# Optimization experiments

Hardware: AMD Instinct MI355X
Metric: run time of the kernel (lower is better)

Reference implementation:

```python
import jax, jax.numpy as jnp
import numpy as np
import math

B, H, T, DH, D = 1, 8, 2048, 64, 64
NEG_INF = -1e30
EPS = 1e-9

def setup_inputs() -> dict:
    key = jax.random.key(0)
    ks = jax.random.split(key, 6)
    q = jax.random.normal(ks[0], (B, H, T, DH), dtype=jnp.float32)
    k = jax.random.normal(ks[1], (B, H, T, DH), dtype=jnp.float32)
    v = jax.random.normal(ks[2], (B, H, T, DH), dtype=jnp.float32)
    edge_type_bias = 0.1 * jax.random.normal(ks[3], (4,), dtype=jnp.float32)
    neigh_idx = jax.random.randint(ks[4], (H, T, D), 0, T).astype(jnp.int32)
    edge_type = jax.random.randint(ks[5], (H, T, D), 0, 5).astype(jnp.int32)
    return {"q": q, "k": k, "v": v, "edge_type_bias": edge_type_bias,
            "neigh_idx": neigh_idx, "edge_type": edge_type}

def _masked_softmax(scores, mask):
    # scores: [B,H,T,D] fp32, mask: [1,H,T,D] bool; zeros on all-masked rows
    masked = jnp.where(mask, scores, NEG_INF)
    m = jnp.max(masked, axis=-1, keepdims=True)
    e = jnp.where(mask, jnp.exp(masked - m), 0.0)
    denom = jnp.maximum(jnp.sum(e, axis=-1, keepdims=True), EPS)
    return e / denom

def reference(q, k, v, edge_type_bias, neigh_idx, edge_type):
    Bq, Hq, Tq, dh = q.shape
    # safe_neighbor_idx: clamp to valid range
    s_idx = jnp.clip(neigh_idx, 0, Tq - 1)                       # [H,T,D]
    # causal_neighbor_mask: valid (>=0) and neighbor <= query position
    pos = jnp.arange(Tq, dtype=neigh_idx.dtype)[None, :, None]    # [1,T,1]
    mask = (neigh_idx >= 0) & (neigh_idx <= pos)                  # [H,T,D]
    # edge-type bias: type 0 -> no bias, types 1..4 -> learnable bias
    full_bias = jnp.concatenate([jnp.zeros((1,), jnp.float32),
                                 edge_type_bias.astype(jnp.float32)])
    bias_htd = full_bias[edge_type]                               # [H,T,D]
    # gather neighbor K/V: k_g[b,h,t,n,:] = k[b,h,s_idx[h,t,n],:]
    h_ix = jnp.arange(Hq)[:, None, None]                          # [H,1,1]
    k_g = k[:, h_ix, s_idx]                                       # [B,H,T,D,dh]
    v_g = v[:, h_ix, s_idx]                                       # [B,H,T,D,dh]
    scores = jnp.einsum('bhtc,bhtnc->bhtn',
                        q.astype(jnp.float32),
                        k_g.astype(jnp.float32)) / math.sqrt(dh)
    scores = scores + bias_htd[None]                              # [B,H,T,D]
    w = _masked_softmax(scores, mask[None])                       # [B,H,T,D]
    y = jnp.einsum('bhtn,bhtnc->bhtc', w, v_g.astype(jnp.float32))
    return y.astype(v.dtype)
```

## Files before the change

### kernel.cpp

```cpp
#include <hip/hip_runtime.h>
#include <hip/hip_fp16.h>

constexpr int H  = 8;
constexpr int T  = 2048;
constexpr int DH = 64;
constexpr int D  = 64;
constexpr int NKV = H * T * DH;

typedef _Float16 half2v __attribute__((ext_vector_type(2)));

#if defined(__has_builtin)
#if __has_builtin(__builtin_amdgcn_fdot2)
#define HAVE_FDOT2 1
#endif
#if __has_builtin(__builtin_amdgcn_permlane32_swap)
#define HAVE_PL32 1
#endif
#if __has_builtin(__builtin_amdgcn_permlane16_swap)
#define HAVE_PL16 1
#endif
#endif

__device__ __forceinline__ float dot2acc(half2v a, half2v b, float c) {
#ifdef HAVE_FDOT2
    return __builtin_amdgcn_fdot2(a, b, c, false);
#else
    return c + (float)a.x * (float)b.x + (float)a.y * (float)b.y;
#endif
}

__device__ __forceinline__ half2v h2bits(int b) { return __builtin_bit_cast(half2v, b); }

__device__ __forceinline__ half2v f2h2(float x, float y) {
    __half2 h = __float22half2_rn(make_float2(x, y));
    return __builtin_bit_cast(half2v, h);
}

template<int CTRL>
__device__ __forceinline__ float dpp_mov_f(float x) {
    int yi = __builtin_amdgcn_update_dpp(0, __builtin_bit_cast(int, x),
                                         CTRL, 0xF, 0xF, true);
    return __builtin_bit_cast(float, yi);
}
template<int CTRL>
__device__ __forceinline__ float dpp_add_f(float x) { return x + dpp_mov_f<CTRL>(x); }
template<int CTRL>
__device__ __forceinline__ float dpp_max_f(float x) { return fmaxf(x, dpp_mov_f<CTRL>(x)); }

__device__ __forceinline__ float xor32add_f(float x) {
#ifdef HAVE_PL32
    unsigned u = __builtin_bit_cast(unsigned, x);
    auto r = __builtin_amdgcn_permlane32_swap(u, u, false, false);
    return __builtin_bit_cast(float, (unsigned)r[0]) + __builtin_bit_cast(float, (unsigned)r[1]);
#else
    return x + __shfl_xor(x, 32);
#endif
}
__device__ __forceinline__ float xor32max_f(float x) {
#ifdef HAVE_PL32
    unsigned u = __builtin_bit_cast(unsigned, x);
    auto r = __builtin_amdgcn_permlane32_swap(u, u, false, false);
    return fmaxf(__builtin_bit_cast(float, (unsigned)r[0]), __builtin_bit_cast(float, (unsigned)r[1]));
#else
    return fmaxf(x, __shfl_xor(x, 32));
#endif
}
__device__ __forceinline__ float xor16add_f(float x) {
#ifdef HAVE_PL16
    unsigned u = __builtin_bit_cast(unsigned, x);
    auto r = __builtin_amdgcn_permlane16_swap(u, u, false, false);
    return __builtin_bit_cast(float, (unsigned)r[0]) + __builtin_bit_cast(float, (unsigned)r[1]);
#else
    return x + __shfl_xor(x, 16);
#endif
}
__device__ __forceinline__ float xor16max_f(float x) {
#ifdef HAVE_PL16
    unsigned u = __builtin_bit_cast(unsigned, x);
    auto r = __builtin_amdgcn_permlane16_swap(u, u, false, false);
    return fmaxf(__builtin_bit_cast(float, (unsigned)r[0]), __builtin_bit_cast(float, (unsigned)r[1]));
#else
    return fmaxf(x, __shfl_xor(x, 16));
#endif
}
__device__ __forceinline__ half2v xor32add_h2(half2v x) {
#ifdef HAVE_PL32
    unsigned u = __builtin_bit_cast(unsigned, x);
    auto r = __builtin_amdgcn_permlane32_swap(u, u, false, false);
    return h2bits((int)r[0]) + h2bits((int)r[1]);
#else
    return x + h2bits(__shfl_xor(__builtin_bit_cast(int, x), 32));
#endif
}
__device__ __forceinline__ half2v xor16add_h2(half2v x) {
#ifdef HAVE_PL16
    unsigned u = __builtin_bit_cast(unsigned, x);
    auto r = __builtin_amdgcn_permlane16_swap(u, u, false, false);
    return h2bits((int)r[0]) + h2bits((int)r[1]);
#else
    return x + h2bits(__shfl_xor(__builtin_bit_cast(int, x), 16));
#endif
}
__device__ __forceinline__ half2v xor8add_h2(half2v x) {
    return x + h2bits(__shfl_xor(__builtin_bit_cast(int, x), 8));
}

__global__ __launch_bounds__(256) void cvt_f32_f16(
    const float* __restrict__ k, const float* __restrict__ v,
    __half* __restrict__ kh, __half* __restrict__ vh)
{
    const int i = (blockIdx.x * 256 + threadIdx.x) * 8;
    const float* src = (blockIdx.y == 0) ? k : v;
    __half*      dst = (blockIdx.y == 0) ? kh : vh;
    const float4 a = *reinterpret_cast<const float4*>(src + i);
    const float4 b = *reinterpret_cast<const float4*>(src + i + 4);
    __half2 hh[4];
    hh[0] = __float22half2_rn(make_float2(a.x, a.y));
    hh[1] = __float22half2_rn(make_float2(a.z, a.w));
    hh[2] = __float22half2_rn(make_float2(b.x, b.y));
    hh[3] = __float22half2_rn(make_float2(b.z, b.w));
    *reinterpret_cast<float4*>(dst + i) = *reinterpret_cast<const float4*>(hh);
}

__global__ __launch_bounds__(256) void wayfinder_attn_f16(
    const float* __restrict__ q,
    const __half* __restrict__ kh,
    const __half* __restrict__ vh,
    const float* __restrict__ eb,
    const int*   __restrict__ nidx,
    const int*   __restrict__ etyp,
    float* __restrict__ out)
{
    const int wave = threadIdx.x >> 6;
    const int lane = threadIdx.x & 63;
    const int bid  = blockIdx.x;
    const int work = ((bid & 7) << 9) | (bid >> 3);
    const int flat = (work << 2) + wave;
    const int h    = flat >> 11;
    const int t    = flat & (T - 1);
    const int grp  = lane >> 3;
    const int sub  = lane & 7;

    const long long rowoff = (long long)flat * DH;
    const int*      nrow   = nidx + (long long)flat * D;
    const int*      erow   = etyp + (long long)flat * D;

    const int4 i0 = *reinterpret_cast<const int4*>(nrow + grp * 8);
    const int4 i1 = *reinterpret_cast<const int4*>(nrow + grp * 8 + 4);
    const int4 e0 = *reinterpret_cast<const int4*>(erow + grp * 8);
    const int4 e1 = *reinterpret_cast<const int4*>(erow + grp * 8 + 4);

    const float4 qa = *reinterpret_cast<const float4*>(q + rowoff + sub * 8);
    const float4 qb = *reinterpret_cast<const float4*>(q + rowoff + sub * 8 + 4);

    const int idx_i[8] = {i0.x, i0.y, i0.z, i0.w, i1.x, i1.y, i1.z, i1.w};
    const int et_i [8] = {e0.x, e0.y, e0.z, e0.w, e1.x, e1.y, e1.z, e1.w};

    const __half* khead = kh + (long long)h * T * DH;
    const __half* vhead = vh + (long long)h * T * DH;

    int s_i[8];
    int mskbits = 0;
    #pragma unroll
    for (int i = 0; i < 8; ++i) {
        const bool mk = (unsigned)idx_i[i] <= (unsigned)t;
        s_i[i] = mk ? idx_i[i] : 0;
        mskbits |= mk ? (1 << i) : 0;
    }

    float4 kf[8], vf[8];
    #pragma unroll
    for (int i = 0; i < 8; ++i) {
        const long long ro = (long long)s_i[i] * DH + sub * 8;
        kf[i] = *reinterpret_cast<const float4*>(khead + ro);
        vf[i] = *reinterpret_cast<const float4*>(vhead + ro);
    }

    const float4 ebv = *reinterpret_cast<const float4*>(eb);
    float bias_i[8];
    #pragma unroll
    for (int i = 0; i < 8; ++i) {
        const int et = et_i[i];
        bias_i[i] = (et == 1) ? ebv.x : (et == 2) ? ebv.y :
                    (et == 3) ? ebv.z : (et == 4) ? ebv.w : 0.0f;
    }

    half2v qp[4];
    qp[0] = f2h2(qa.x, qa.y);
    qp[1] = f2h2(qa.z, qa.w);
    qp[2] = f2h2(qb.x, qb.y);
    qp[3] = f2h2(qb.z, qb.w);

    float sc[8];
    #pragma unroll
    for (int i = 0; i < 8; ++i) {
        const half2v* kp = reinterpret_cast<const half2v*>(&kf[i]);
        float p = dot2acc(qp[0], kp[0],
                  dot2acc(qp[1], kp[1],
                  dot2acc(qp[2], kp[2],
                  dot2acc(qp[3], kp[3], 0.0f))));
        p = dpp_add_f<0xB1>(p);
        p = dpp_add_f<0x4E>(p);
        p = dpp_add_f<0x141>(p);
        sc[i] = p;
    }

    float masked[8];
    float mx = -1e30f;
    #pragma unroll
    for (int i = 0; i < 8; ++i) {
        const bool mk = (mskbits >> i) & 1;
        masked[i] = mk ? fmaf(sc[i], 0.125f, bias_i[i]) : -1e30f;
        mx = fmaxf(mx, masked[i]);
    }
    mx = dpp_max_f<0x140>(mx);
    mx = xor16max_f(mx);
    mx = xor32max_f(mx);

    float e[8];
    float sum = 0.0f;
    #pragma unroll
    for (int i = 0; i < 8; ++i) {
        const bool mk = (mskbits >> i) & 1;
        e[i] = mk ? __expf(masked[i] - mx) : 0.0f;
        sum += e[i];
    }
    sum = dpp_add_f<0x140>(sum);
    sum = xor16add_f(sum);
    sum = xor32add_f(sum);
    const float rden = 1.0f / fmaxf(sum, 1e-9f);

    float acc[8] = {0.f, 0.f, 0.f, 0.f, 0.f, 0.f, 0.f, 0.f};
    #pragma unroll
    for (int i = 0; i < 8; ++i) {
        const float w = e[i] * rden;
        const half2v* vp = reinterpret_cast<const half2v*>(&vf[i]);
        acc[0] += w * (float)vp[0].x;  acc[1] += w * (float)vp[0].y;
        acc[2] += w * (float)vp[1].x;  acc[3] += w * (float)vp[1].y;
        acc[4] += w * (float)vp[2].x;  acc[5] += w * (float)vp[2].y;
        acc[6] += w * (float)vp[3].x;  acc[7] += w * (float)vp[3].y;
    }

    half2v h0 = f2h2(acc[0], acc[1]);
    half2v h1 = f2h2(acc[2], acc[3]);
    half2v h2 = f2h2(acc[4], acc[5]);
    half2v h3 = f2h2(acc[6], acc[7]);
    h0 = xor8add_h2(h0);  h1 = xor8add_h2(h1);
    h2 = xor8add_h2(h2);  h3 = xor8add_h2(h3);
    h0 = xor16add_h2(h0); h1 = xor16add_h2(h1);
    h2 = xor16add_h2(h2); h3 = xor16add_h2(h3);
    h0 = xor32add_h2(h0); h1 = xor32add_h2(h1);
    h2 = xor32add_h2(h2); h3 = xor32add_h2(h3);

    if (lane < 16) {
        const int s8   = (lane & 7) * 8;
        const int half = lane >> 3;
        const float4 o = half
            ? make_float4((float)h2.x, (float)h2.y, (float)h3.x, (float)h3.y)
            : make_float4((float)h0.x, (float)h0.y, (float)h1.x, (float)h1.y);
        *reinterpret_cast<float4*>(out + rowoff + s8 + half * 4) = o;
    }
}

__global__ __launch_bounds__(256) void wayfinder_attn_f32(
    const float* __restrict__ q, const float* __restrict__ k,
    const float* __restrict__ v, const float* __restrict__ eb,
    const int* __restrict__ nidx, const int* __restrict__ etyp,
    float* __restrict__ out)
{
    const int wave = threadIdx.x >> 6;
    const int lane = threadIdx.x & 63;
    const int flat = (blockIdx.x << 2) + wave;
    const int h    = flat >> 11;
    const int t    = flat & (T - 1);
    const int grp  = lane >> 4;
    const int sub  = lane & 15;

    __shared__ int    sidx[4][64];
    __shared__ float  ssc [4][64];
    __shared__ float2 swv [4][64];

    const long long rowoff = (long long)flat * DH;
    const long long noff = (long long)flat * D + lane;
    const int  idx = nidx[noff];
    const int  et  = etyp[noff];
    const int  s   = min(max(idx, 0), T - 1);
    const bool msk = (idx >= 0) && (idx <= t);
    const float4 ebv  = *reinterpret_cast<const float4*>(eb);
    const float  bias = (et == 1) ? ebv.x : (et == 2) ? ebv.y :
                        (et == 3) ? ebv.z : (et == 4) ? ebv.w : 0.0f;
    sidx[wave][lane] = s;
    const float4 qf = *reinterpret_cast<const float4*>(q + rowoff + sub * 4);
    __syncthreads();

    const float* khead = k + (long long)h * T * DH;
    #pragma unroll
    for (int i = 0; i < 16; ++i) {
        const int n  = i * 4 + grp;
        const int sn = sidx[wave][n];
        const float4 kf = *reinterpret_cast<const float4*>(khead + sn * DH + sub * 4);
        float p = qf.x * kf.x + qf.y * kf.y + qf.z * kf.z + qf.w * kf.w;
        p += __shfl_xor(p, 1);
        p += __shfl_xor(p, 2);
        p += __shfl_xor(p, 4);
        p += __shfl_xor(p, 8);
        if (sub == 0) ssc[wave][n] = p;
    }
    __syncthreads();

    const float sc     = ssc[wave][lane];
    const float masked = msk ? (sc * 0.125f + bias) : -1e30f;
    float mx = masked;
    #pragma unroll
    for (int off = 32; off > 0; off >>= 1) mx = fmaxf(mx, __shfl_xor(mx, off));
    const float e = msk ? __expf(masked - mx) : 0.0f;
    float sum = e;
    #pragma unroll
    for (int off = 32; off > 0; off >>= 1) sum += __shfl_xor(sum, off);
    const float w = e / fmaxf(sum, 1e-9f);
    swv[wave][lane] = make_float2(w, __int_as_float(s));
    __syncthreads();

    const float* vhead = v + (long long)h * T * DH;
    float4 acc = make_float4(0.f, 0.f, 0.f, 0.f);
    #pragma unroll
    for (int i = 0; i < 16; ++i) {
        const int    n  = i * 4 + grp;
        const float2 ws = swv[wave][n];
        const int    sn = __float_as_int(ws.y);
        const float4 vf = *reinterpret_cast<const float4*>(vhead + sn * DH + sub * 4);
        acc.x += ws.x * vf.x; acc.y += ws.x * vf.y;
        acc.z += ws.x * vf.z; acc.w += ws.x * vf.w;
    }
    #pragma unroll
    for (int off = 16; off <= 32; off <<= 1) {
        acc.x += __shfl_xor(acc.x, off); acc.y += __shfl_xor(acc.y, off);
        acc.z += __shfl_xor(acc.z, off); acc.w += __shfl_xor(acc.w, off);
    }
    if (lane < 16)
        *reinterpret_cast<float4*>(out + rowoff + sub * 4) = acc;
}

extern "C" void kernel_launch(void* const* d_in, const int* in_sizes, int n_in,
                              void* d_out, int out_size, void* d_ws, size_t ws_size,
                              hipStream_t stream) {
    const float* q    = (const float*)d_in[0];
    const float* k    = (const float*)d_in[1];
    const float* v    = (const float*)d_in[2];
    const float* eb   = (const float*)d_in[3];
    const int*   nidx = (const int*)d_in[4];
    const int*   etyp = (const int*)d_in[5];
    float* out = (float*)d_out;

    const size_t need = (size_t)2 * NKV * sizeof(__half);
    if (ws_size >= need) {
        __half* kh = (__half*)d_ws;
        __half* vh = kh + NKV;
        dim3 cgrid(NKV / (256 * 8), 2);
        hipLaunchKernelGGL(cvt_f32_f16, cgrid, dim3(256), 0, stream, k, v, kh, vh);
        hipLaunchKernelGGL(wayfinder_attn_f16, dim3(H * T / 4), dim3(256), 0, stream,
                           q, kh, vh, eb, nidx, etyp, out);
    } else {
        hipLaunchKernelGGL(wayfinder_attn_f32, dim3(H * T / 4), dim3(256), 0, stream,
                           q, k, v, eb, nidx, etyp, out);
    }
}
```

Before: 26.47 us.

## Split each query's neighbor set across two waves with LDS softmax merge

Each query row is now handled by two waves, each covering 32 of the 64 neighbors. Each wave keeps only 4 K/V gathers per lane instead of 8, computes a partial max, sum and output, and the pair is merged through shared memory with a rescaled combine, flash-style. The grid doubles and launch bounds request 8 blocks per unit to raise occupancy and memory-level parallelism. In exchange it adds a block-wide barrier, LDS traffic, duplicated q loads and extra cross-lane reductions.

```diff
diff --git a/kernel.cpp b/kernel.cpp
--- a/kernel.cpp
+++ b/kernel.cpp
@@ -122,7 +122,7 @@
     *reinterpret_cast<float4*>(dst + i) = *reinterpret_cast<const float4*>(hh);
 }
 
-__global__ __launch_bounds__(256) void wayfinder_attn_f16(
+__global__ __launch_bounds__(256, 8) void wayfinder_attn_f16(
     const float* __restrict__ q,
     const __half* __restrict__ kh,
     const __half* __restrict__ vh,
@@ -131,55 +131,58 @@
     const int*   __restrict__ etyp,
     float* __restrict__ out)
 {
+    __shared__ float  sm_m[2][2];
+    __shared__ float  sm_s[2][2];
+    __shared__ float4 sm_o[2][2][16];
+
     const int wave = threadIdx.x >> 6;
     const int lane = threadIdx.x & 63;
+    const int qsel = wave >> 1;
+    const int hlf  = wave & 1;
     const int bid  = blockIdx.x;
-    const int work = ((bid & 7) << 9) | (bid >> 3);
-    const int flat = (work << 2) + wave;
+    const int work = ((bid & 7) << 10) | (bid >> 3);
+    const int flat = (work << 1) | qsel;
     const int h    = flat >> 11;
     const int t    = flat & (T - 1);
     const int grp  = lane >> 3;
     const int sub  = lane & 7;
 
     const long long rowoff = (long long)flat * DH;
-    const int*      nrow   = nidx + (long long)flat * D;
-    const int*      erow   = etyp + (long long)flat * D;
-
-    const int4 i0 = *reinterpret_cast<const int4*>(nrow + grp * 8);
-    const int4 i1 = *reinterpret_cast<const int4*>(nrow + grp * 8 + 4);
-    const int4 e0 = *reinterpret_cast<const int4*>(erow + grp * 8);
-    const int4 e1 = *reinterpret_cast<const int4*>(erow + grp * 8 + 4);
+    const int nbase = hlf * 32 + grp * 4;
+
+    const int4 iv = *reinterpret_cast<const int4*>(nidx + (long long)flat * D + nbase);
+    const int4 ev = *reinterpret_cast<const int4*>(etyp + (long long)flat * D + nbase);
 
     const float4 qa = *reinterpret_cast<const float4*>(q + rowoff + sub * 8);
     const float4 qb = *reinterpret_cast<const float4*>(q + rowoff + sub * 8 + 4);
 
-    const int idx_i[8] = {i0.x, i0.y, i0.z, i0.w, i1.x, i1.y, i1.z, i1.w};
-    const int et_i [8] = {e0.x, e0.y, e0.z, e0.w, e1.x, e1.y, e1.z, e1.w};
+    const int idx_i[4] = {iv.x, iv.y, iv.z, iv.w};
+    const int et_i [4] = {ev.x, ev.y, ev.z, ev.w};
 
     const __half* khead = kh + (long long)h * T * DH;
     const __half* vhead = vh + (long long)h * T * DH;
 
-    int s_i[8];
+    int s_i[4];
     int mskbits = 0;
     #pragma unroll
-    for (int i = 0; i < 8; ++i) {
+    for (int i = 0; i < 4; ++i) {
         const bool mk = (unsigned)idx_i[i] <= (unsigned)t;
         s_i[i] = mk ? idx_i[i] : 0;
         mskbits |= mk ? (1 << i) : 0;
     }
 
-    float4 kf[8], vf[8];
-    #pragma unroll
-    for (int i = 0; i < 8; ++i) {
+    float4 kf[4], vf[4];
+    #pragma unroll
+    for (int i = 0; i < 4; ++i) {
         const long long ro = (long long)s_i[i] * DH + sub * 8;
         kf[i] = *reinterpret_cast<const float4*>(khead + ro);
         vf[i] = *reinterpret_cast<const float4*>(vhead + ro);
     }
 
     const float4 ebv = *reinterpret_cast<const float4*>(eb);
-    float bias_i[8];
-    #pragma unroll
-    for (int i = 0; i < 8; ++i) {
+    float bias_i[4];
+    #pragma unroll
+    for (int i = 0; i < 4; ++i) {
         const int et = et_i[i];
         bias_i[i] = (et == 1) ? ebv.x : (et == 2) ? ebv.y :
                     (et == 3) ? ebv.z : (et == 4) ? ebv.w : 0.0f;
@@ -191,9 +194,9 @@
     qp[2] = f2h2(qb.x, qb.y);
     qp[3] = f2h2(qb.z, qb.w);
 
-    float sc[8];
-    #pragma unroll
-    for (int i = 0; i < 8; ++i) {
+    float sc[4];
+    #pragma unroll
+    for (int i = 0; i < 4; ++i) {
         const half2v* kp = reinterpret_cast<const half2v*>(&kf[i]);
         float p = dot2acc(qp[0], kp[0],
                   dot2acc(qp[1], kp[1],
@@ -205,10 +208,10 @@
         sc[i] = p;
     }
 
-    float masked[8];
+    float masked[4];
     float mx = -1e30f;
     #pragma unroll
-    for (int i = 0; i < 8; ++i) {
+    for (int i = 0; i < 4; ++i) {
         const bool mk = (mskbits >> i) & 1;
         masked[i] = mk ? fmaf(sc[i], 0.125f, bias_i[i]) : -1e30f;
         mx = fmaxf(mx, masked[i]);
@@ -217,10 +220,10 @@
     mx = xor16max_f(mx);
     mx = xor32max_f(mx);
 
-    float e[8];
+    float e[4];
     float sum = 0.0f;
     #pragma unroll
-    for (int i = 0; i < 8; ++i) {
+    for (int i = 0; i < 4; ++i) {
         const bool mk = (mskbits >> i) & 1;
         e[i] = mk ? __expf(masked[i] - mx) : 0.0f;
         sum += e[i];
@@ -228,12 +231,11 @@
     sum = dpp_add_f<0x140>(sum);
     sum = xor16add_f(sum);
     sum = xor32add_f(sum);
-    const float rden = 1.0f / fmaxf(sum, 1e-9f);
 
     float acc[8] = {0.f, 0.f, 0.f, 0.f, 0.f, 0.f, 0.f, 0.f};
     #pragma unroll
-    for (int i = 0; i < 8; ++i) {
-        const float w = e[i] * rden;
+    for (int i = 0; i < 4; ++i) {
+        const float w = e[i];
         const half2v* vp = reinterpret_cast<const half2v*>(&vf[i]);
         acc[0] += w * (float)vp[0].x;  acc[1] += w * (float)vp[0].y;
         acc[2] += w * (float)vp[1].x;  acc[3] += w * (float)vp[1].y;
@@ -252,13 +254,32 @@
     h0 = xor32add_h2(h0); h1 = xor32add_h2(h1);
     h2 = xor32add_h2(h2); h3 = xor32add_h2(h3);
 
+    if (lane == 0) { sm_m[qsel][hlf] = mx; sm_s[qsel][hlf] = sum; }
     if (lane < 16) {
-        const int s8   = (lane & 7) * 8;
-        const int half = lane >> 3;
-        const float4 o = half
+        const int halfo = lane >> 3;
+        sm_o[qsel][hlf][lane] = halfo
             ? make_float4((float)h2.x, (float)h2.y, (float)h3.x, (float)h3.y)
             : make_float4((float)h0.x, (float)h0.y, (float)h1.x, (float)h1.y);
-        *reinterpret_cast<float4*>(out + rowoff + s8 + half * 4) = o;
+    }
+    __syncthreads();
+
+    if (hlf == 0 && lane < 16) {
+        const float m0 = sm_m[qsel][0], s0 = sm_s[qsel][0];
+        const float m1 = sm_m[qsel][1], s1 = sm_s[qsel][1];
+        const float m  = fmaxf(m0, m1);
+        const float f0 = __expf(m0 - m);
+        const float f1 = __expf(m1 - m);
+        const float r  = 1.0f / fmaxf(s0 * f0 + s1 * f1, 1e-9f);
+        const float4 o0 = sm_o[qsel][0][lane];
+        const float4 o1 = sm_o[qsel][1][lane];
+        float4 o;
+        o.x = (o0.x * f0 + o1.x * f1) * r;
+        o.y = (o0.y * f0 + o1.y * f1) * r;
+        o.z = (o0.z * f0 + o1.z * f1) * r;
+        o.w = (o0.w * f0 + o1.w * f1) * r;
+        const int s8    = (lane & 7) * 8;
+        const int halfo = lane >> 3;
+        *reinterpret_cast<float4*>(out + rowoff + s8 + halfo * 4) = o;
     }
 }
 
@@ -358,7 +379,7 @@
         __half* vh = kh + NKV;
         dim3 cgrid(NKV / (256 * 8), 2);
         hipLaunchKernelGGL(cvt_f32_f16, cgrid, dim3(256), 0, stream, k, v, kh, vh);
-        hipLaunchKernelGGL(wayfinder_attn_f16, dim3(H * T / 4), dim3(256), 0, stream,
+        hipLaunchKernelGGL(wayfinder_attn_f16, dim3(H * T / 2), dim3(256), 0, stream,
                            q, kh, vh, eb, nidx, etyp, out);
     } else {
         hipLaunchKernelGGL(wayfinder_attn_f32, dim3(H * T / 4), dim3(256), 0, stream,
```

After: 26.51 us. About the same (+0.1%).
